# Performance work log

Measured on AMD Instinct MI355X. Metric: run time of the kernel, lower is better.

## Reference

```python
import jax, jax.numpy as jnp
import numpy as np

B, T, N, F = 16, 12, 1000, 64
K_CHEB, OUT = 3, 64


def setup_inputs() -> dict:
    key = jax.random.key(0)
    k1, k2, k3, k4 = jax.random.split(key, 4)
    x = jax.random.normal(k1, (B, T, N, F), dtype=jnp.float32)
    SAtt = jax.random.uniform(k2, (B, N, N), dtype=jnp.float32)
    cheb = jax.random.normal(k3, (K_CHEB, N, N), dtype=jnp.float32) * 0.05
    Theta = jax.random.normal(k4, (K_CHEB, F, OUT), dtype=jnp.float32) * 0.05
    return {"x": x, "SAtt": SAtt, "cheb": cheb, "Theta": Theta}


def reference(x, SAtt, cheb, Theta):
    # Attention-masked Chebyshev polynomials: A[b,k,i,j] = cheb[k,i,j] * SAtt[b,i,j]
    A = cheb[None, :, :, :] * SAtt[:, None, :, :]          # (B,K,N,N)
    # rhs[b,t,k,i,f] = sum_j A[b,k,j,i] * x[b,t,j,f]  (transpose of A in original code)
    rhs = jnp.einsum('bkji,btjf->btkif', A, x)             # (B,T,K,N,F)
    # accumulate over k with per-k feature transform Theta[k]
    out = jnp.einsum('btkif,kfo->btio', rhs, Theta)        # (B,T,N,OUT)
    return jax.nn.relu(out)
```

## Files before the change

### kernel.cpp

```cpp
#include <hip/hip_runtime.h>

#define B_  16
#define T_  12
#define N_  1000
#define F_  64
#define KC  3
#define O_  64
#define NP  1024
#define KP  (KC * NP)
#define CC  (T_ * O_)

typedef __bf16 bf16x8 __attribute__((ext_vector_type(8)));
typedef float  f32x4  __attribute__((ext_vector_type(4)));

__device__ __forceinline__ unsigned short f2bf(float f) {
  __bf16 h = (__bf16)f;
  return __builtin_bit_cast(unsigned short, h);
}

__device__ __forceinline__ void gl_lds16(const void* g, void* l) {
  __builtin_amdgcn_global_load_lds(
      (const __attribute__((address_space(1))) unsigned int*)g,
      (__attribute__((address_space(3))) unsigned int*)l,
      16, 0, 0);
}

__global__ __launch_bounds__(256) void k_build_as(
    const float* __restrict__ SAtt, const float* __restrict__ cheb,
    unsigned short* __restrict__ ASt) {
  __shared__ unsigned short prod[KC][64][66];
  const int tid = threadIdx.x;
  const int ib = blockIdx.x * 64, jb = blockIdx.y * 64;

  const int ii4 = (tid & 15) * 4, jr = tid >> 4;
  const int gi = ib + ii4;
  const bool iok = gi < N_;

  float4 ch[4][KC];
  int gjc[4];
  bool okm[4];
#pragma unroll
  for (int p = 0; p < 4; ++p) {
    const int gj = jb + p * 16 + jr;
    gjc[p] = gj < N_ ? gj : N_ - 1;
    okm[p] = iok && (gj < N_);
#pragma unroll
    for (int k = 0; k < KC; ++k) {
      ch[p][k] = make_float4(0.f, 0.f, 0.f, 0.f);
      if (iok)
        ch[p][k] = *(const float4*)&cheb[((size_t)k * N_ + gjc[p]) * N_ + gi];
    }
  }

  const int j8 = (tid & 7) * 8, i0 = tid >> 3;

  for (int bb = 0; bb < 8; ++bb) {
    const int b = blockIdx.z * 8 + bb;
    const float* sb = SAtt + (size_t)b * N_ * N_;
    if (bb) __syncthreads();
#pragma unroll
    for (int p = 0; p < 4; ++p) {
      const int jj = p * 16 + jr;
      float4 s4 = make_float4(0.f, 0.f, 0.f, 0.f);
      if (iok) s4 = *(const float4*)&sb[(size_t)gjc[p] * N_ + gi];
#pragma unroll
      for (int k = 0; k < KC; ++k) {
        ushort2 lo, hi;
        lo.x = okm[p] ? f2bf(ch[p][k].x * s4.x) : (unsigned short)0;
        lo.y = okm[p] ? f2bf(ch[p][k].y * s4.y) : (unsigned short)0;
        hi.x = okm[p] ? f2bf(ch[p][k].z * s4.z) : (unsigned short)0;
        hi.y = okm[p] ? f2bf(ch[p][k].w * s4.w) : (unsigned short)0;
        *(ushort2*)&prod[k][jj][ii4]     = lo;
        *(ushort2*)&prod[k][jj][ii4 + 2] = hi;
      }
    }
    __syncthreads();
#pragma unroll
    for (int pp = 0; pp < 2; ++pp) {
      const int iw = pp * 32 + i0;
#pragma unroll
      for (int k = 0; k < KC; ++k) {
        unsigned short v[8];
#pragma unroll
        for (int m = 0; m < 8; ++m) v[m] = prod[k][j8 + m][iw];
        *(uint4*)&ASt[((size_t)(b * NP + ib + iw) * KC + k) * NP + jb + j8] =
            *(uint4*)v;
      }
    }
  }
}

__global__ __launch_bounds__(256) void k_build_y(
    const float* __restrict__ x, const float* __restrict__ Theta,
    unsigned short* __restrict__ Yt) {
  __shared__ unsigned short thl[KC][64][72];
  __shared__ unsigned short xl[128][72];
  __shared__ unsigned short ot[64][136];
  const int tid = threadIdx.x;
  const int jb = blockIdx.x * 128;

#pragma unroll
  for (int it = 0; it < 12; ++it) {
    const int e = (tid + it * 256) * 4;
    const int k = e >> 12, f = (e >> 6) & 63, o0 = e & 63;
    const float4 v = *(const float4*)&Theta[e];
    thl[k][o0 + 0][f] = f2bf(v.x);
    thl[k][o0 + 1][f] = f2bf(v.y);
    thl[k][o0 + 2][f] = f2bf(v.z);
    thl[k][o0 + 3][f] = f2bf(v.w);
  }

  const int w = tid >> 6, l = tid & 63, quad = l >> 4, lr = l & 15;
  const int o16 = tid >> 4, j8v = (tid & 15) * 8;

  for (int tt = 0; tt < 3; ++tt) {
    const int bt = blockIdx.y * T_ + blockIdx.z * 3 + tt;
    const float* xrow = x + ((size_t)bt * N_ + jb) * F_;
#pragma unroll
    for (int p = 0; p < 8; ++p) {
      const int i4 = tid + p * 256;
      const int fl = i4 * 4, j = fl >> 6, f = fl & 63;
      float4 v;
      if (jb + j < N_) v = ((const float4*)xrow)[i4];
      else             v = make_float4(0.f, 0.f, 0.f, 0.f);
      ushort4 u;
      u.x = f2bf(v.x); u.y = f2bf(v.y); u.z = f2bf(v.z); u.w = f2bf(v.w);
      *(ushort4*)&xl[j][f] = u;
    }
    __syncthreads();

#pragma unroll
    for (int k = 0; k < KC; ++k) {
      f32x4 acc[4][2];
#pragma unroll
      for (int mi = 0; mi < 4; ++mi)
#pragma unroll
        for (int ni = 0; ni < 2; ++ni)
          acc[mi][ni] = (f32x4){0.f, 0.f, 0.f, 0.f};
#pragma unroll
      for (int ks = 0; ks < 2; ++ks) {
        const int fo = ks * 32 + quad * 8;
        bf16x8 a[4], bb[2];
#pragma unroll
        for (int mi = 0; mi < 4; ++mi)
          a[mi] = *(const bf16x8*)&thl[k][mi * 16 + lr][fo];
#pragma unroll
        for (int ni = 0; ni < 2; ++ni)
          bb[ni] = *(const bf16x8*)&xl[w * 32 + ni * 16 + lr][fo];
#pragma unroll
        for (int mi = 0; mi < 4; ++mi)
#pragma unroll
          for (int ni = 0; ni < 2; ++ni)
            acc[mi][ni] = __builtin_amdgcn_mfma_f32_16x16x32_bf16(
                a[mi], bb[ni], acc[mi][ni], 0, 0, 0);
      }
      __syncthreads();
#pragma unroll
      for (int mi = 0; mi < 4; ++mi)
#pragma unroll
        for (int ni = 0; ni < 2; ++ni)
#pragma unroll
          for (int r = 0; r < 4; ++r)
            ot[mi * 16 + quad * 4 + r][w * 32 + ni * 16 + lr] =
                f2bf(acc[mi][ni][r]);
      __syncthreads();
#pragma unroll
      for (int oo = 0; oo < 4; ++oo) {
        const int o = oo * 16 + o16;
        const uint4 v = *(const uint4*)&ot[o][j8v];
        *(uint4*)&Yt[((size_t)(bt * O_ + o) * KC + k) * NP + jb + j8v] = v;
      }
    }
  }
}

__global__ __launch_bounds__(256, 2) void k_gemm(
    const unsigned short* __restrict__ ASt, const unsigned short* __restrict__ Yt,
    float* __restrict__ out) {
  __shared__ unsigned short Al[128 * 64];
  __shared__ unsigned short Bl[128 * 64];
  const int tid = threadIdx.x;
  const int bid = blockIdx.x;
  const int xcd = bid & 7, s = bid >> 3;
  const int b = xcd * 2 + (s / 48);
  const int r48 = s % 48;
  const int ib = (r48 / 6) * 128, cb = (r48 % 6) * 128;

  const unsigned short* Abase = ASt + ((size_t)b * NP + ib) * KP;
  const unsigned short* Bbase = Yt + ((size_t)b * CC + cb) * KP;
  const int w = tid >> 6, l = tid & 63, quad = l >> 4, lr = l & 15;
  const int wr = w & 1, wc = w >> 1;
  const int lrow = l >> 3, lchunk = l & 7;
  const int src_chunk = lchunk ^ lrow;
  const int p0 = quad ^ (lr & 7);

  f32x4 acc[4][4];
#pragma unroll
  for (int mi = 0; mi < 4; ++mi)
#pragma unroll
    for (int ci = 0; ci < 4; ++ci)
      acc[mi][ci] = (f32x4){0.f, 0.f, 0.f, 0.f};

  for (int kt = 0; kt < KP / 64; ++kt) {
    __syncthreads();
    const int k0 = kt * 64;
#pragma unroll
    for (int s4 = 0; s4 < 4; ++s4) {
      const int row = w * 32 + s4 * 8;
      gl_lds16(Abase + (size_t)(row + lrow) * KP + k0 + src_chunk * 8,
               &Al[row * 64]);
      gl_lds16(Bbase + (size_t)(row + lrow) * KP + k0 + src_chunk * 8,
               &Bl[row * 64]);
    }
    __syncthreads();
#pragma unroll
    for (int ks = 0; ks < 2; ++ks) {
      const int pc = (p0 ^ (ks * 4)) * 8;
      bf16x8 a[4], bb[4];
#pragma unroll
      for (int mi = 0; mi < 4; ++mi)
        a[mi] = *(const bf16x8*)&Al[(wr * 64 + mi * 16 + lr) * 64 + pc];
#pragma unroll
      for (int ci = 0; ci < 4; ++ci)
        bb[ci] = *(const bf16x8*)&Bl[(wc * 64 + ci * 16 + lr) * 64 + pc];
#pragma unroll
      for (int mi = 0; mi < 4; ++mi)
#pragma unroll
        for (int ci = 0; ci < 4; ++ci)
          acc[mi][ci] = __builtin_amdgcn_mfma_f32_16x16x32_bf16(
              a[mi], bb[ci], acc[mi][ci], 0, 0, 0);
    }
  }

#pragma unroll
  for (int mi = 0; mi < 4; ++mi) {
    const int i = ib + wr * 64 + mi * 16 + quad * 4;
#pragma unroll
    for (int ci = 0; ci < 4; ++ci) {
      const int c = cb + wc * 64 + ci * 16 + lr;
      const int t = c >> 6, o = c & 63;
#pragma unroll
      for (int r = 0; r < 4; ++r) {
        if (i + r < N_) {
          const float v = acc[mi][ci][r];
          out[((size_t)(b * T_ + t) * N_ + (i + r)) * O_ + o] = v > 0.f ? v : 0.f;
        }
      }
    }
  }
}

extern "C" void kernel_launch(void* const* d_in, const int* in_sizes, int n_in,
                              void* d_out, int out_size, void* d_ws, size_t ws_size,
                              hipStream_t stream) {
  const float* x     = (const float*)d_in[0];
  const float* SAtt  = (const float*)d_in[1];
  const float* cheb  = (const float*)d_in[2];
  const float* Theta = (const float*)d_in[3];
  float* out = (float*)d_out;

  unsigned short* ASt = (unsigned short*)d_ws;
  unsigned short* Yt  = ASt + (size_t)B_ * NP * KC * NP;

  k_build_as<<<dim3(16, 16, 2), 256, 0, stream>>>(SAtt, cheb, ASt);
  k_build_y<<<dim3(8, B_, 4), 256, 0, stream>>>(x, Theta, Yt);
  k_gemm<<<768, 256, 0, stream>>>(ASt, Yt, out);
}
```

Before: 308.8 us.

## Fuse x·Theta projection into the main GEMM, dropping the Yt intermediate

The separate k_build_y kernel and its Yt workspace are removed. Each GEMM block now loads its x tile, converts it to bf16 in LDS, and computes the Theta projection with MFMA into the B tile for every (j-tile, k) step. This avoids writing and re-reading a large bf16 intermediate and one kernel launch. The cost is redundant projection work: each of the 8 row-blocks per (b, column-block) recomputes the same Y tile. It also adds LDS use (extra xs and thl buffers), which may limit occupancy at 2 blocks per CU.

```diff
diff --git a/kernel.cpp b/kernel.cpp
--- a/kernel.cpp
+++ b/kernel.cpp
@@ -90,14 +90,30 @@
   }
 }
 
-__global__ __launch_bounds__(256) void k_build_y(
-    const float* __restrict__ x, const float* __restrict__ Theta,
-    unsigned short* __restrict__ Yt) {
+__global__ __launch_bounds__(256, 2) void k_gemm(
+    const unsigned short* __restrict__ ASt, const float* __restrict__ x,
+    const float* __restrict__ Theta, float* __restrict__ out) {
+  __shared__ unsigned short Al[128 * 64];
+  __shared__ unsigned short Bl[128 * 64];
+  __shared__ unsigned short xs[128 * 64];
   __shared__ unsigned short thl[KC][64][72];
-  __shared__ unsigned short xl[128][72];
-  __shared__ unsigned short ot[64][136];
+
   const int tid = threadIdx.x;
-  const int jb = blockIdx.x * 128;
+  const int bid = blockIdx.x;
+  const int xcd = bid & 7, s = bid >> 3;
+  const int b = xcd * 2 + (s / 48);
+  const int r48 = s % 48;
+  const int ib = (r48 / 6) * 128, cb = (r48 % 6) * 128;
+  const int t0 = cb >> 6;
+  const int bt0 = b * T_ + t0;
+
+  const unsigned short* Abase = ASt + ((size_t)b * NP + ib) * KP;
+  const int w = tid >> 6, l = tid & 63, quad = l >> 4, lr = l & 15;
+  const int wr = w & 1, wc = w >> 1;
+  const int lrow = l >> 3, lchunk = l & 7;
+  const int src_chunk = lchunk ^ lrow;
+  const int p0 = quad ^ (lr & 7);
+  const int ytt = w & 1, yjh = w >> 1;
 
 #pragma unroll
   for (int it = 0; it < 12; ++it) {
@@ -110,125 +126,98 @@
     thl[k][o0 + 3][f] = f2bf(v.w);
   }
 
-  const int w = tid >> 6, l = tid & 63, quad = l >> 4, lr = l & 15;
-  const int o16 = tid >> 4, j8v = (tid & 15) * 8;
-
-  for (int tt = 0; tt < 3; ++tt) {
-    const int bt = blockIdx.y * T_ + blockIdx.z * 3 + tt;
-    const float* xrow = x + ((size_t)bt * N_ + jb) * F_;
+  f32x4 acc[4][4];
+#pragma unroll
+  for (int mi = 0; mi < 4; ++mi)
+#pragma unroll
+    for (int ci = 0; ci < 4; ++ci)
+      acc[mi][ci] = (f32x4){0.f, 0.f, 0.f, 0.f};
+
+#pragma unroll 1
+  for (int jt = 0; jt < 16; ++jt) {
+    const int j0 = jt * 64;
 #pragma unroll
     for (int p = 0; p < 8; ++p) {
-      const int i4 = tid + p * 256;
-      const int fl = i4 * 4, j = fl >> 6, f = fl & 63;
-      float4 v;
-      if (jb + j < N_) v = ((const float4*)xrow)[i4];
-      else             v = make_float4(0.f, 0.f, 0.f, 0.f);
+      const int idx = tid + p * 256;
+      const int f4 = idx & 15, j = (idx >> 4) & 63, tt = idx >> 10;
+      const int jg = j0 + j;
+      float4 v = make_float4(0.f, 0.f, 0.f, 0.f);
+      if (jg < N_)
+        v = *(const float4*)&x[((size_t)(bt0 + tt) * N_ + jg) * F_ + f4 * 4];
       ushort4 u;
       u.x = f2bf(v.x); u.y = f2bf(v.y); u.z = f2bf(v.z); u.w = f2bf(v.w);
-      *(ushort4*)&xl[j][f] = u;
-    }
-    __syncthreads();
-
-#pragma unroll
+      const int rr = tt * 64 + j;
+      const int off = rr * 64 + (((f4 >> 1) ^ (rr & 7)) * 8) + (f4 & 1) * 4;
+      *(ushort4*)&xs[off] = u;
+    }
+
+#pragma unroll 1
     for (int k = 0; k < KC; ++k) {
-      f32x4 acc[4][2];
-#pragma unroll
-      for (int mi = 0; mi < 4; ++mi)
-#pragma unroll
-        for (int ni = 0; ni < 2; ++ni)
-          acc[mi][ni] = (f32x4){0.f, 0.f, 0.f, 0.f};
+      __syncthreads();
+      const int koff = k * NP + j0;
+#pragma unroll
+      for (int s4 = 0; s4 < 4; ++s4) {
+        const int row = w * 32 + s4 * 8;
+        gl_lds16(Abase + (size_t)(row + lrow) * KP + koff + src_chunk * 8,
+                 &Al[row * 64]);
+      }
+      f32x4 yac[2][4];
+#pragma unroll
+      for (int j2 = 0; j2 < 2; ++j2)
+#pragma unroll
+        for (int ot = 0; ot < 4; ++ot)
+          yac[j2][ot] = (f32x4){0.f, 0.f, 0.f, 0.f};
 #pragma unroll
       for (int ks = 0; ks < 2; ++ks) {
-        const int fo = ks * 32 + quad * 8;
-        bf16x8 a[4], bb[2];
+        bf16x8 xa[2], tb[4];
+#pragma unroll
+        for (int j2 = 0; j2 < 2; ++j2) {
+          const int rr = ytt * 64 + yjh * 32 + j2 * 16 + lr;
+          xa[j2] = *(const bf16x8*)
+              &xs[rr * 64 + (((ks * 4 + quad) ^ (rr & 7)) * 8)];
+        }
+#pragma unroll
+        for (int ot = 0; ot < 4; ++ot)
+          tb[ot] = *(const bf16x8*)&thl[k][ot * 16 + lr][ks * 32 + quad * 8];
+#pragma unroll
+        for (int j2 = 0; j2 < 2; ++j2)
+#pragma unroll
+          for (int ot = 0; ot < 4; ++ot)
+            yac[j2][ot] = __builtin_amdgcn_mfma_f32_16x16x32_bf16(
+                xa[j2], tb[ot], yac[j2][ot], 0, 0, 0);
+      }
+#pragma unroll
+      for (int j2 = 0; j2 < 2; ++j2) {
+        const int jloc4 = yjh * 32 + j2 * 16 + quad * 4;
+#pragma unroll
+        for (int ot = 0; ot < 4; ++ot) {
+          const int crow = ytt * 64 + ot * 16 + lr;
+          ushort4 u;
+          u.x = f2bf(yac[j2][ot][0]); u.y = f2bf(yac[j2][ot][1]);
+          u.z = f2bf(yac[j2][ot][2]); u.w = f2bf(yac[j2][ot][3]);
+          const int off =
+              crow * 64 + (((jloc4 >> 3) ^ (crow & 7)) * 8) + (jloc4 & 7);
+          *(ushort4*)&Bl[off] = u;
+        }
+      }
+      __syncthreads();
+#pragma unroll
+      for (int ks = 0; ks < 2; ++ks) {
+        const int pc = (p0 ^ (ks * 4)) * 8;
+        bf16x8 a[4], bb[4];
 #pragma unroll
         for (int mi = 0; mi < 4; ++mi)
-          a[mi] = *(const bf16x8*)&thl[k][mi * 16 + lr][fo];
-#pragma unroll
-        for (int ni = 0; ni < 2; ++ni)
-          bb[ni] = *(const bf16x8*)&xl[w * 32 + ni * 16 + lr][fo];
+          a[mi] = *(const bf16x8*)&Al[(wr * 64 + mi * 16 + lr) * 64 + pc];
+#pragma unroll
+        for (int ci = 0; ci < 4; ++ci)
+          bb[ci] = *(const bf16x8*)&Bl[(wc * 64 + ci * 16 + lr) * 64 + pc];
 #pragma unroll
         for (int mi = 0; mi < 4; ++mi)
 #pragma unroll
-          for (int ni = 0; ni < 2; ++ni)
-            acc[mi][ni] = __builtin_amdgcn_mfma_f32_16x16x32_bf16(
-                a[mi], bb[ni], acc[mi][ni], 0, 0, 0);
-      }
-      __syncthreads();
-#pragma unroll
-      for (int mi = 0; mi < 4; ++mi)
-#pragma unroll
-        for (int ni = 0; ni < 2; ++ni)
-#pragma unroll
-          for (int r = 0; r < 4; ++r)
-            ot[mi * 16 + quad * 4 + r][w * 32 + ni * 16 + lr] =
-                f2bf(acc[mi][ni][r]);
-      __syncthreads();
-#pragma unroll
-      for (int oo = 0; oo < 4; ++oo) {
-        const int o = oo * 16 + o16;
-        const uint4 v = *(const uint4*)&ot[o][j8v];
-        *(uint4*)&Yt[((size_t)(bt * O_ + o) * KC + k) * NP + jb + j8v] = v;
-      }
-    }
-  }
-}
-
-__global__ __launch_bounds__(256, 2) void k_gemm(
-    const unsigned short* __restrict__ ASt, const unsigned short* __restrict__ Yt,
-    float* __restrict__ out) {
-  __shared__ unsigned short Al[128 * 64];
-  __shared__ unsigned short Bl[128 * 64];
-  const int tid = threadIdx.x;
-  const int bid = blockIdx.x;
-  const int xcd = bid & 7, s = bid >> 3;
-  const int b = xcd * 2 + (s / 48);
-  const int r48 = s % 48;
-  const int ib = (r48 / 6) * 128, cb = (r48 % 6) * 128;
-
-  const unsigned short* Abase = ASt + ((size_t)b * NP + ib) * KP;
-  const unsigned short* Bbase = Yt + ((size_t)b * CC + cb) * KP;
-  const int w = tid >> 6, l = tid & 63, quad = l >> 4, lr = l & 15;
-  const int wr = w & 1, wc = w >> 1;
-  const int lrow = l >> 3, lchunk = l & 7;
-  const int src_chunk = lchunk ^ lrow;
-  const int p0 = quad ^ (lr & 7);
-
-  f32x4 acc[4][4];
-#pragma unroll
-  for (int mi = 0; mi < 4; ++mi)
-#pragma unroll
-    for (int ci = 0; ci < 4; ++ci)
-      acc[mi][ci] = (f32x4){0.f, 0.f, 0.f, 0.f};
-
-  for (int kt = 0; kt < KP / 64; ++kt) {
-    __syncthreads();
-    const int k0 = kt * 64;
-#pragma unroll
-    for (int s4 = 0; s4 < 4; ++s4) {
-      const int row = w * 32 + s4 * 8;
-      gl_lds16(Abase + (size_t)(row + lrow) * KP + k0 + src_chunk * 8,
-               &Al[row * 64]);
-      gl_lds16(Bbase + (size_t)(row + lrow) * KP + k0 + src_chunk * 8,
-               &Bl[row * 64]);
-    }
-    __syncthreads();
-#pragma unroll
-    for (int ks = 0; ks < 2; ++ks) {
-      const int pc = (p0 ^ (ks * 4)) * 8;
-      bf16x8 a[4], bb[4];
-#pragma unroll
-      for (int mi = 0; mi < 4; ++mi)
-        a[mi] = *(const bf16x8*)&Al[(wr * 64 + mi * 16 + lr) * 64 + pc];
-#pragma unroll
-      for (int ci = 0; ci < 4; ++ci)
-        bb[ci] = *(const bf16x8*)&Bl[(wc * 64 + ci * 16 + lr) * 64 + pc];
-#pragma unroll
-      for (int mi = 0; mi < 4; ++mi)
-#pragma unroll
-        for (int ci = 0; ci < 4; ++ci)
-          acc[mi][ci] = __builtin_amdgcn_mfma_f32_16x16x32_bf16(
-              a[mi], bb[ci], acc[mi][ci], 0, 0, 0);
+          for (int ci = 0; ci < 4; ++ci)
+            acc[mi][ci] = __builtin_amdgcn_mfma_f32_16x16x32_bf16(
+                a[mi], bb[ci], acc[mi][ci], 0, 0, 0);
+      }
     }
   }
 
@@ -260,9 +249,7 @@
   float* out = (float*)d_out;
 
   unsigned short* ASt = (unsigned short*)d_ws;
-  unsigned short* Yt  = ASt + (size_t)B_ * NP * KC * NP;
 
   k_build_as<<<dim3(16, 16, 2), 256, 0, stream>>>(SAtt, cheb, ASt);
-  k_build_y<<<dim3(8, B_, 4), 256, 0, stream>>>(x, Theta, Yt);
-  k_gemm<<<768, 256, 0, stream>>>(ASt, Yt, out);
-}
+  k_gemm<<<768, 256, 0, stream>>>(ASt, x, Theta, out);
+}
```

Result: slower. 379.4 us (+22.9%).
